# Performance work log

Measured on AMD Instinct MI355X. Metric: run time of the kernel, lower is better.

The kernel has to match this reference:

```python
import jax, jax.numpy as jnp
import numpy as np

B, T, D, H, E, O = 4, 2048, 512, 2048, 4, 512
C = 1024  # expert capacity
HE = H // E  # per-expert hidden width


def setup_inputs() -> dict:
    key = jax.random.key(0)
    ks = jax.random.split(key, 7)
    x = jax.random.normal(ks[0], (B, T, D), dtype=jnp.float32)
    dispatch_mask = jax.random.uniform(ks[1], (B, T, E, C), dtype=jnp.float32)
    combine_array = jax.random.uniform(ks[2], (B, T, E, C), dtype=jnp.float32)
    # per-expert parameters (fc1 contract, fc2 expand)
    w1 = jax.random.normal(ks[3], (E, D, HE), dtype=jnp.float32) * (1.0 / np.sqrt(D))
    b1 = jnp.zeros((E, HE), dtype=jnp.float32)
    w2 = jax.random.normal(ks[4], (E, HE, O), dtype=jnp.float32) * (1.0 / np.sqrt(HE))
    b2 = jnp.zeros((O,), dtype=jnp.float32)
    return {"x": x, "dispatch_mask": dispatch_mask, "combine_array": combine_array,
            "w1": w1, "b1": b1, "w2": w2, "b2": b2}


def reference(x, dispatch_mask, combine_array, w1, b1, w2, b2):
    # dispatch: gather tokens into per-expert capacity buffers [B,E,C,D]
    xd = jnp.einsum('btd,btec->becd', x, dispatch_mask)
    # per-expert fc1: [B,E,C,HE]
    h = jnp.einsum('becd,edh->bech', xd, w1) + b1[None, :, None, :]
    # GELU (exact erf form, matching torch nn.GELU default); norm/dropout are identity
    h = jax.nn.gelu(h, approximate=False)
    # per-expert fc2: [B,E,C,O]
    y = jnp.einsum('bech,eho->beco', h, w2)
    # combine: scatter expert outputs back to tokens [B,T,O]
    out = jnp.einsum('beco,btec->bto', y, combine_array) + b2
    return out
```

## Files before the change

### kernel.cpp

```cpp
#include <hip/hip_runtime.h>
#include <math.h>

namespace {

typedef short short8 __attribute__((ext_vector_type(8)));
typedef int i32x4 __attribute__((ext_vector_type(4)));
typedef float f32x4 __attribute__((ext_vector_type(4)));

constexpr int kB = 4, kT = 2048, kD = 512, kE = 4, kC = 1024, kHE = 512,
              kO = 512, kEC = 4096;

__device__ __forceinline__ unsigned short f2bf(float f) {
    unsigned int u = __float_as_uint(f);
    u += 0x7fffu + ((u >> 16) & 1u);
    return (unsigned short)(u >> 16);
}

__device__ __forceinline__ float gelu_exact(float v) {
    return 0.5f * v * (1.0f + erff(v * 0.70710678118654752f));
}

#define GLDS16(g, l)                                                      \
    __builtin_amdgcn_global_load_lds(                                     \
        (const __attribute__((address_space(1))) unsigned int*)(g),       \
        (__attribute__((address_space(3))) unsigned int*)(l), 16, 0, 0)

__global__ __launch_bounds__(256)
void transpose_cast(const float* __restrict__ in, unsigned short* __restrict__ out,
                    int R, int Cc, long long sIn, long long sOut)
{
    __shared__ float tile[32][33];
    const int z = blockIdx.z;
    const float* ip = in + (long long)z * sIn;
    unsigned short* op = out + (long long)z * sOut;
    const int c0 = blockIdx.x * 32, r0 = blockIdx.y * 32;
    const int tx = threadIdx.x & 31, ty = threadIdx.x >> 5;
#pragma unroll
    for (int i = 0; i < 4; ++i) {
        const int r = ty + i * 8;
        tile[r][tx] = ip[(size_t)(r0 + r) * Cc + c0 + tx];
    }
    __syncthreads();
#pragma unroll
    for (int i = 0; i < 4; ++i) {
        const int c = ty + i * 8;
        op[(size_t)(c0 + c) * R + r0 + tx] = f2bf(tile[tx][c]);
    }
}

__global__ __launch_bounds__(256)
void cast_bf16(const float* __restrict__ in, unsigned short* __restrict__ out,
               long long n)
{
    const long long i = ((long long)blockIdx.x * blockDim.x + threadIdx.x) * 4;
    if (i < n) {
        const float4 v = *(const float4*)&in[i];
        unsigned short o[4] = {f2bf(v.x), f2bf(v.y), f2bf(v.z), f2bf(v.w)};
        *(uint2*)&out[i] = *(const uint2*)o;
    }
}

template <int MODE>
__global__ __launch_bounds__(256, 1)
void mfma_gemm(const unsigned short* __restrict__ Aall,
               const unsigned short* __restrict__ Ball,
               const float* __restrict__ biasAll,
               void* __restrict__ Call,
               int M, int N, int K,
               long long sA, long long sB, long long sC,
               int zModA, int zModB, int zModBias, int biasStride, int bShift)
{
    __shared__ unsigned short As[4][128 * 64];
    __shared__ unsigned short Bs[4][128 * 64];

    const int z = blockIdx.z;
    const unsigned short* Ab = Aall + (long long)(z % zModA) * sA;
    const unsigned short* Bb = Ball + (long long)(z % zModB) * sB;
    const float* bias =
        (MODE != 0) ? biasAll + (long long)(z % zModBias) * biasStride : nullptr;

    const int gx = gridDim.x;
    int lin = blockIdx.y * gx + blockIdx.x;
    const int nwg = gx * gridDim.y;
    if ((nwg & 7) == 0) {
        const int q = nwg >> 3;
        lin = (lin & 7) * q + (lin >> 3);
    }
    const int gxs = 31 - __clz(gx);
    const int bx = lin & (gx - 1);
    const int by = lin >> gxs;
    const int row0 = by * 128;
    const int colB = bx * 128;

    const int t = threadIdx.x;
    const int lane = t & 63;
    const int w = t >> 6;
    const int wrow = w * 32;
    const int l8r = lane >> 3;
    const int l8c = ((lane & 7) ^ l8r) * 8;

    const int wm = (w >> 1) * 64;
    const int wn = (w & 1) * 64;
    const int fr = lane & 15;
    const int fq = (lane >> 4) * 8;
    const int fsw = (fr & 7) * 8;

    const unsigned int bMask = (1u << bShift) - 1u;

    f32x4 acc[4][4] = {};

    const unsigned aB0 =
        (unsigned)(size_t)(const __attribute__((address_space(3))) unsigned short*)
            &As[0][0] +
        (unsigned)(((wm + fr) * 64 + (fq ^ fsw)) * 2);
    const unsigned bB0 =
        (unsigned)(size_t)(const __attribute__((address_space(3))) unsigned short*)
            &Bs[0][0] +
        (unsigned)(((wn + fr) * 64 + (fq ^ fsw)) * 2);

    struct FragSet { i32x4 a0[4], a1[4], b0[4], b1[4]; };
    FragSet R0, R1;

#define DSR0(d, a) asm volatile("ds_read_b128 %0, %1" : "=v"(d) : "v"(a))
#define DSR1(d, a) asm volatile("ds_read_b128 %0, %1 offset:2048" : "=v"(d) : "v"(a))
#define DSR2(d, a) asm volatile("ds_read_b128 %0, %1 offset:4096" : "=v"(d) : "v"(a))
#define DSR3(d, a) asm volatile("ds_read_b128 %0, %1 offset:6144" : "=v"(d) : "v"(a))

#define READ16(R, CB)                                                         \
    do {                                                                      \
        const unsigned A0c = aB0 + (CB) * 16384u, A1c = A0c ^ 64u;            \
        const unsigned B0c = bB0 + (CB) * 16384u, B1c = B0c ^ 64u;            \
        DSR0(R.a0[0], A0c); DSR1(R.a0[1], A0c); DSR2(R.a0[2], A0c); DSR3(R.a0[3], A0c); \
        DSR0(R.b0[0], B0c); DSR1(R.b0[1], B0c); DSR2(R.b0[2], B0c); DSR3(R.b0[3], B0c); \
        DSR0(R.a1[0], A1c); DSR1(R.a1[1], A1c); DSR2(R.a1[2], A1c); DSR3(R.a1[3], A1c); \
        DSR0(R.b1[0], B1c); DSR1(R.b1[1], B1c); DSR2(R.b1[2], B1c); DSR3(R.b1[3], B1c); \
    } while (0)

#define MFMA16(R)                                                             \
    do {                                                                      \
        _Pragma("unroll") for (int i_ = 0; i_ < 4; ++i_)                      \
            _Pragma("unroll") for (int j_ = 0; j_ < 4; ++j_)                  \
                acc[i_][j_] = __builtin_amdgcn_mfma_f32_16x16x32_bf16(        \
                    __builtin_bit_cast(short8, R.a0[i_]),                     \
                    __builtin_bit_cast(short8, R.b0[j_]), acc[i_][j_], 0, 0, 0); \
        _Pragma("unroll") for (int i_ = 0; i_ < 4; ++i_)                      \
            _Pragma("unroll") for (int j_ = 0; j_ < 4; ++j_)                  \
                acc[i_][j_] = __builtin_amdgcn_mfma_f32_16x16x32_bf16(        \
                    __builtin_bit_cast(short8, R.a1[i_]),                     \
                    __builtin_bit_cast(short8, R.b1[j_]), acc[i_][j_], 0, 0, 0); \
    } while (0)

#define STAGE(buf, k0)                                                        \
    do {                                                                      \
        _Pragma("unroll")                                                     \
        for (int r = 0; r < 4; ++r) {                                         \
            const int ar = row0 + wrow + r * 8 + l8r;                         \
            GLDS16(Ab + (size_t)ar * K + ((k0) + l8c),                        \
                   &As[buf][(wrow + r * 8) * 64]);                            \
            const int bn = colB + wrow + r * 8 + l8r;                         \
            const int gk = (k0) + l8c;                                        \
            const size_t boff =                                               \
                (((size_t)(gk >> bShift) * N + bn) << bShift) + (gk & bMask); \
            GLDS16(Bb + boff, &Bs[buf][(wrow + r * 8) * 64]);                 \
        }                                                                     \
    } while (0)

#define ITER_FULL(T, CBRD, CBST, Rmf, Rrd)                                    \
    do {                                                                      \
        STAGE(CBST, ((T) + 2) * 64);                                          \
        asm volatile("s_waitcnt vmcnt(8)" ::: "memory");                      \
        __builtin_amdgcn_s_barrier();                                         \
        READ16(Rrd, CBRD);                                                    \
        MFMA16(Rmf);                                                          \
        asm volatile("s_waitcnt lgkmcnt(0)" ::: "memory");                    \
        __builtin_amdgcn_sched_barrier(0);                                    \
    } while (0)

    const int nt = K / 64;

    STAGE(0, 0);
    STAGE(1, 64);
    asm volatile("s_waitcnt vmcnt(8)" ::: "memory");
    __builtin_amdgcn_s_barrier();
    READ16(R0, 0);
    asm volatile("s_waitcnt lgkmcnt(0)" ::: "memory");
    __builtin_amdgcn_sched_barrier(0);

    for (int t0 = 0; t0 + 4 < nt; t0 += 4) {
        ITER_FULL(t0 + 0, 1, 2, R0, R1);
        ITER_FULL(t0 + 1, 2, 3, R1, R0);
        ITER_FULL(t0 + 2, 3, 0, R0, R1);
        ITER_FULL(t0 + 3, 0, 1, R1, R0);
    }
    ITER_FULL(nt - 4, 1, 2, R0, R1);
    ITER_FULL(nt - 3, 2, 3, R1, R0);
    asm volatile("s_waitcnt vmcnt(0)" ::: "memory");
    __builtin_amdgcn_s_barrier();
    READ16(R1, 3);
    MFMA16(R0);
    asm volatile("s_waitcnt lgkmcnt(0)" ::: "memory");
    __builtin_amdgcn_sched_barrier(0);
    MFMA16(R1);

#undef ITER_FULL
#undef STAGE
#undef MFMA16
#undef READ16
#undef DSR0
#undef DSR1
#undef DSR2
#undef DSR3

    const long long cz = (long long)z * sC;
#pragma unroll
    for (int i = 0; i < 4; ++i) {
        const int rowb = row0 + wm + i * 16 + (lane >> 4) * 4;
#pragma unroll
        for (int j = 0; j < 4; ++j) {
            const int col = colB + wn + j * 16 + fr;
            const float bv = (MODE != 0) ? bias[col] : 0.0f;
#pragma unroll
            for (int r = 0; r < 4; ++r) {
                const float v = acc[i][j][r];
                const size_t idx = (size_t)cz + (size_t)(rowb + r) * N + col;
                if (MODE == 0)
                    ((unsigned short*)Call)[idx] = f2bf(v);
                else if (MODE == 1)
                    ((unsigned short*)Call)[idx] = f2bf(gelu_exact(v + bv));
                else
                    ((float*)Call)[idx] = v + bv;
            }
        }
    }
}

}

extern "C" void kernel_launch(void* const* d_in, const int* in_sizes, int n_in,
                              void* d_out, int out_size, void* d_ws, size_t ws_size,
                              hipStream_t stream)
{
    const float* x    = (const float*)d_in[0];
    const float* mask = (const float*)d_in[1];
    const float* comb = (const float*)d_in[2];
    const float* w1   = (const float*)d_in[3];
    const float* b1   = (const float*)d_in[4];
    const float* w2   = (const float*)d_in[5];
    const float* b2   = (const float*)d_in[6];
    float* out = (float*)d_out;

    unsigned short* ws    = (unsigned short*)d_ws;
    unsigned short* regA  = ws;
    unsigned short* xT    = regA + 33554432;
    unsigned short* w1T   = xT + 4194304;
    unsigned short* w2T   = w1T + 1048576;
    unsigned short* xd    = w2T + 1048576;
    unsigned short* h     = xd + 8388608;
    unsigned short* maskT = regA;
    unsigned short* combB = regA;
    unsigned short* yT    = xd;

    dim3 blk(256);

    transpose_cast<<<dim3(kEC / 32, kT / 32, kB), blk, 0, stream>>>(
        mask, maskT, kT, kEC, (long long)kT * kEC, (long long)kT * kEC);
    transpose_cast<<<dim3(kD / 32, kT / 32, kB), blk, 0, stream>>>(
        x, xT, kT, kD, (long long)kT * kD, (long long)kT * kD);
    transpose_cast<<<dim3(kHE / 32, kD / 32, kE), blk, 0, stream>>>(
        w1, w1T, kD, kHE, (long long)kD * kHE, (long long)kD * kHE);
    transpose_cast<<<dim3(kO / 32, kHE / 32, kE), blk, 0, stream>>>(
        w2, w2T, kHE, kO, (long long)kHE * kO, (long long)kHE * kO);

    mfma_gemm<0><<<dim3(kD / 128, kEC / 128, kB), blk, 0, stream>>>(
        maskT, xT, nullptr, xd, kEC, kD, kT,
        (long long)kEC * kT, (long long)kD * kT, (long long)kEC * kD,
        kB, kB, 1, 0, 11);

    cast_bf16<<<dim3(33554432 / 4 / 256), blk, 0, stream>>>(
        comb, combB, 33554432LL);

    mfma_gemm<1><<<dim3(kHE / 128, kC / 128, kB * kE), blk, 0, stream>>>(
        xd, w1T, b1, h, kC, kHE, kD,
        (long long)kC * kD, (long long)kHE * kD, (long long)kC * kHE,
        kB * kE, kE, kE, kHE, 9);

    mfma_gemm<0><<<dim3(kC / 128, kO / 128, kB * kE), blk, 0, stream>>>(
        w2T, h, nullptr, yT, kO, kC, kHE,
        (long long)kO * kHE, (long long)kC * kHE, (long long)kO * kC,
        kE, kB * kE, 1, 0, 9);

    mfma_gemm<3><<<dim3(kO / 128, kT / 128, kB), blk, 0, stream>>>(
        combB, yT, b2, out, kT, kO, kEC,
        (long long)kT * kEC, (long long)kE * kO * kC, (long long)kT * kO,
        kB, kB, 1, 0, 10);
}
```

Measured before the change: 442.9 us.

## Fuse input conversions into one launch and deepen GEMM prefetch to three stages

Merges the four transpose-cast kernels and, when the workspace is large enough, the combine-array cast into a single flat-grid kernel. This removes several launches and the serialization between them. It also changes the 4-buffer LDS ring in the MFMA GEMM from a prefetch distance of two tiles to three, with adjusted vmcnt waits and a new epilogue, to hide more global-load latency. The fused path relies on a separate combB buffer, so it only runs when the workspace size check passes. Otherwise it falls back to the old cast kernel.

```diff
diff --git a/kernel.cpp b/kernel.cpp
--- a/kernel.cpp
+++ b/kernel.cpp
@@ -25,15 +25,11 @@
         (const __attribute__((address_space(1))) unsigned int*)(g),       \
         (__attribute__((address_space(3))) unsigned int*)(l), 16, 0, 0)
 
-__global__ __launch_bounds__(256)
-void transpose_cast(const float* __restrict__ in, unsigned short* __restrict__ out,
-                    int R, int Cc, long long sIn, long long sOut)
-{
-    __shared__ float tile[32][33];
-    const int z = blockIdx.z;
-    const float* ip = in + (long long)z * sIn;
-    unsigned short* op = out + (long long)z * sOut;
-    const int c0 = blockIdx.x * 32, r0 = blockIdx.y * 32;
+__device__ __forceinline__ void tc_body(float (*tile)[33],
+                                        const float* __restrict__ ip,
+                                        unsigned short* __restrict__ op,
+                                        int R, int Cc, int c0, int r0)
+{
     const int tx = threadIdx.x & 31, ty = threadIdx.x >> 5;
 #pragma unroll
     for (int i = 0; i < 4; ++i) {
@@ -45,6 +41,43 @@
     for (int i = 0; i < 4; ++i) {
         const int c = ty + i * 8;
         op[(size_t)(c0 + c) * R + r0 + tx] = f2bf(tile[tx][c]);
+    }
+}
+
+__global__ __launch_bounds__(256)
+void convert_all(const float* __restrict__ mask, unsigned short* __restrict__ maskT,
+                 const float* __restrict__ x, unsigned short* __restrict__ xT,
+                 const float* __restrict__ w1, unsigned short* __restrict__ w1T,
+                 const float* __restrict__ w2, unsigned short* __restrict__ w2T,
+                 const float* __restrict__ comb, unsigned short* __restrict__ combB)
+{
+    __shared__ float tile[32][33];
+    const int bid = blockIdx.x;
+    if (bid < 32768) {
+        const int txi = bid & 127, tyi = (bid >> 7) & 63, z = bid >> 13;
+        tc_body(tile, mask + (long long)z * kT * kEC,
+                maskT + (long long)z * kT * kEC, kT, kEC, txi * 32, tyi * 32);
+    } else if (bid < 36864) {
+        const int b2 = bid - 32768;
+        const int txi = b2 & 15, tyi = (b2 >> 4) & 63, z = b2 >> 10;
+        tc_body(tile, x + (long long)z * kT * kD,
+                xT + (long long)z * kT * kD, kT, kD, txi * 32, tyi * 32);
+    } else if (bid < 37888) {
+        const int b3 = bid - 36864;
+        const int txi = b3 & 15, tyi = (b3 >> 4) & 15, z = b3 >> 8;
+        tc_body(tile, w1 + (long long)z * kD * kHE,
+                w1T + (long long)z * kD * kHE, kD, kHE, txi * 32, tyi * 32);
+    } else if (bid < 38912) {
+        const int b4 = bid - 37888;
+        const int txi = b4 & 15, tyi = (b4 >> 4) & 15, z = b4 >> 8;
+        tc_body(tile, w2 + (long long)z * kHE * kO,
+                w2T + (long long)z * kHE * kO, kHE, kO, txi * 32, tyi * 32);
+    } else {
+        const long long i =
+            ((long long)(bid - 38912) * 256 + threadIdx.x) * 4;
+        const float4 v = *(const float4*)&comb[i];
+        unsigned short o[4] = {f2bf(v.x), f2bf(v.y), f2bf(v.z), f2bf(v.w)};
+        *(uint2*)&combB[i] = *(const uint2*)o;
     }
 }
 
@@ -167,8 +200,8 @@
 
 #define ITER_FULL(T, CBRD, CBST, Rmf, Rrd)                                    \
     do {                                                                      \
-        STAGE(CBST, ((T) + 2) * 64);                                          \
-        asm volatile("s_waitcnt vmcnt(8)" ::: "memory");                      \
+        STAGE(CBST, ((T) + 3) * 64);                                          \
+        asm volatile("s_waitcnt vmcnt(16)" ::: "memory");                     \
         __builtin_amdgcn_s_barrier();                                         \
         READ16(Rrd, CBRD);                                                    \
         MFMA16(Rmf);                                                          \
@@ -180,20 +213,26 @@
 
     STAGE(0, 0);
     STAGE(1, 64);
-    asm volatile("s_waitcnt vmcnt(8)" ::: "memory");
+    STAGE(2, 128);
+    asm volatile("s_waitcnt vmcnt(16)" ::: "memory");
     __builtin_amdgcn_s_barrier();
     READ16(R0, 0);
     asm volatile("s_waitcnt lgkmcnt(0)" ::: "memory");
     __builtin_amdgcn_sched_barrier(0);
 
-    for (int t0 = 0; t0 + 4 < nt; t0 += 4) {
-        ITER_FULL(t0 + 0, 1, 2, R0, R1);
-        ITER_FULL(t0 + 1, 2, 3, R1, R0);
-        ITER_FULL(t0 + 2, 3, 0, R0, R1);
-        ITER_FULL(t0 + 3, 0, 1, R1, R0);
-    }
-    ITER_FULL(nt - 4, 1, 2, R0, R1);
-    ITER_FULL(nt - 3, 2, 3, R1, R0);
+    for (int t0 = 0; t0 + 7 < nt; t0 += 4) {
+        ITER_FULL(t0 + 0, 1, 3, R0, R1);
+        ITER_FULL(t0 + 1, 2, 0, R1, R0);
+        ITER_FULL(t0 + 2, 3, 1, R0, R1);
+        ITER_FULL(t0 + 3, 0, 2, R1, R0);
+    }
+    ITER_FULL(nt - 4, 1, 3, R0, R1);
+    asm volatile("s_waitcnt vmcnt(8)" ::: "memory");
+    __builtin_amdgcn_s_barrier();
+    READ16(R0, 2);
+    MFMA16(R1);
+    asm volatile("s_waitcnt lgkmcnt(0)" ::: "memory");
+    __builtin_amdgcn_sched_barrier(0);
     asm volatile("s_waitcnt vmcnt(0)" ::: "memory");
     __builtin_amdgcn_s_barrier();
     READ16(R1, 3);
@@ -257,27 +296,25 @@
     unsigned short* xd    = w2T + 1048576;
     unsigned short* h     = xd + 8388608;
     unsigned short* maskT = regA;
-    unsigned short* combB = regA;
     unsigned short* yT    = xd;
 
+    const bool bigWs = ws_size >= (size_t)180355072;
+    unsigned short* combB = bigWs ? (h + 8388608) : regA;
+
     dim3 blk(256);
 
-    transpose_cast<<<dim3(kEC / 32, kT / 32, kB), blk, 0, stream>>>(
-        mask, maskT, kT, kEC, (long long)kT * kEC, (long long)kT * kEC);
-    transpose_cast<<<dim3(kD / 32, kT / 32, kB), blk, 0, stream>>>(
-        x, xT, kT, kD, (long long)kT * kD, (long long)kT * kD);
-    transpose_cast<<<dim3(kHE / 32, kD / 32, kE), blk, 0, stream>>>(
-        w1, w1T, kD, kHE, (long long)kD * kHE, (long long)kD * kHE);
-    transpose_cast<<<dim3(kO / 32, kHE / 32, kE), blk, 0, stream>>>(
-        w2, w2T, kHE, kO, (long long)kHE * kO, (long long)kHE * kO);
+    convert_all<<<dim3(bigWs ? 71680 : 38912), blk, 0, stream>>>(
+        mask, maskT, x, xT, w1, w1T, w2, w2T, comb, combB);
 
     mfma_gemm<0><<<dim3(kD / 128, kEC / 128, kB), blk, 0, stream>>>(
         maskT, xT, nullptr, xd, kEC, kD, kT,
         (long long)kEC * kT, (long long)kD * kT, (long long)kEC * kD,
         kB, kB, 1, 0, 11);
 
-    cast_bf16<<<dim3(33554432 / 4 / 256), blk, 0, stream>>>(
-        comb, combB, 33554432LL);
+    if (!bigWs) {
+        cast_bf16<<<dim3(33554432 / 4 / 256), blk, 0, stream>>>(
+            comb, combB, 33554432LL);
+    }
 
     mfma_gemm<1><<<dim3(kHE / 128, kC / 128, kB * kE), blk, 0, stream>>>(
         xd, w1T, b1, h, kC, kHE, kD,
```

Measured after the change: 461.8 us. 1.04x slower.

## Deepen GEMM prefetch to three stages, interleave LDS reads with MFMAs, widen transpose stores

Applied to the files above, without the earlier changes.

The GEMM main loop now prefetches three K-tiles ahead instead of two, using all four LDS buffers. Each iteration splits the fragment reads into four groups, each followed by eight MFMAs, so LDS latency hides behind matrix math. The transpose kernel now handles 64-row tiles and writes two packed bf16 values per 32-bit store to cut store count. The risks are a more fragile pipeline tail and rigid sched_barriers that may limit the compiler's own scheduling.

```diff
diff --git a/kernel.cpp b/kernel.cpp
--- a/kernel.cpp
+++ b/kernel.cpp
@@ -29,14 +29,14 @@
 void transpose_cast(const float* __restrict__ in, unsigned short* __restrict__ out,
                     int R, int Cc, long long sIn, long long sOut)
 {
-    __shared__ float tile[32][33];
+    __shared__ float tile[64][33];
     const int z = blockIdx.z;
     const float* ip = in + (long long)z * sIn;
     unsigned short* op = out + (long long)z * sOut;
-    const int c0 = blockIdx.x * 32, r0 = blockIdx.y * 32;
+    const int c0 = blockIdx.x * 32, r0 = blockIdx.y * 64;
     const int tx = threadIdx.x & 31, ty = threadIdx.x >> 5;
 #pragma unroll
-    for (int i = 0; i < 4; ++i) {
+    for (int i = 0; i < 8; ++i) {
         const int r = ty + i * 8;
         tile[r][tx] = ip[(size_t)(r0 + r) * Cc + c0 + tx];
     }
@@ -44,7 +44,9 @@
 #pragma unroll
     for (int i = 0; i < 4; ++i) {
         const int c = ty + i * 8;
-        op[(size_t)(c0 + c) * R + r0 + tx] = f2bf(tile[tx][c]);
+        const unsigned lo = f2bf(tile[tx * 2][c]);
+        const unsigned hi = f2bf(tile[tx * 2 + 1][c]);
+        *(unsigned*)&op[(size_t)(c0 + c) * R + r0 + tx * 2] = lo | (hi << 16);
     }
 }
 
@@ -126,28 +128,34 @@
 #define DSR2(d, a) asm volatile("ds_read_b128 %0, %1 offset:4096" : "=v"(d) : "v"(a))
 #define DSR3(d, a) asm volatile("ds_read_b128 %0, %1 offset:6144" : "=v"(d) : "v"(a))
 
+#define READ4(arr, addr)                                                      \
+    do {                                                                      \
+        DSR0((arr)[0], (addr)); DSR1((arr)[1], (addr));                       \
+        DSR2((arr)[2], (addr)); DSR3((arr)[3], (addr));                       \
+    } while (0)
+
+#define MFMA8(Aarr, Barr, ilo)                                                \
+    do {                                                                      \
+        _Pragma("unroll") for (int i_ = (ilo); i_ < (ilo) + 2; ++i_)          \
+            _Pragma("unroll") for (int j_ = 0; j_ < 4; ++j_)                  \
+                acc[i_][j_] = __builtin_amdgcn_mfma_f32_16x16x32_bf16(        \
+                    __builtin_bit_cast(short8, (Aarr)[i_]),                   \
+                    __builtin_bit_cast(short8, (Barr)[j_]), acc[i_][j_],      \
+                    0, 0, 0);                                                 \
+    } while (0)
+
 #define READ16(R, CB)                                                         \
     do {                                                                      \
         const unsigned A0c = aB0 + (CB) * 16384u, A1c = A0c ^ 64u;            \
         const unsigned B0c = bB0 + (CB) * 16384u, B1c = B0c ^ 64u;            \
-        DSR0(R.a0[0], A0c); DSR1(R.a0[1], A0c); DSR2(R.a0[2], A0c); DSR3(R.a0[3], A0c); \
-        DSR0(R.b0[0], B0c); DSR1(R.b0[1], B0c); DSR2(R.b0[2], B0c); DSR3(R.b0[3], B0c); \
-        DSR0(R.a1[0], A1c); DSR1(R.a1[1], A1c); DSR2(R.a1[2], A1c); DSR3(R.a1[3], A1c); \
-        DSR0(R.b1[0], B1c); DSR1(R.b1[1], B1c); DSR2(R.b1[2], B1c); DSR3(R.b1[3], B1c); \
+        READ4(R.a0, A0c); READ4(R.b0, B0c);                                   \
+        READ4(R.a1, A1c); READ4(R.b1, B1c);                                   \
     } while (0)
 
 #define MFMA16(R)                                                             \
     do {                                                                      \
-        _Pragma("unroll") for (int i_ = 0; i_ < 4; ++i_)                      \
-            _Pragma("unroll") for (int j_ = 0; j_ < 4; ++j_)                  \
-                acc[i_][j_] = __builtin_amdgcn_mfma_f32_16x16x32_bf16(        \
-                    __builtin_bit_cast(short8, R.a0[i_]),                     \
-                    __builtin_bit_cast(short8, R.b0[j_]), acc[i_][j_], 0, 0, 0); \
-        _Pragma("unroll") for (int i_ = 0; i_ < 4; ++i_)                      \
-            _Pragma("unroll") for (int j_ = 0; j_ < 4; ++j_)                  \
-                acc[i_][j_] = __builtin_amdgcn_mfma_f32_16x16x32_bf16(        \
-                    __builtin_bit_cast(short8, R.a1[i_]),                     \
-                    __builtin_bit_cast(short8, R.b1[j_]), acc[i_][j_], 0, 0, 0); \
+        MFMA8(R.a0, R.b0, 0); MFMA8(R.a0, R.b0, 2);                           \
+        MFMA8(R.a1, R.b1, 0); MFMA8(R.a1, R.b1, 2);                           \
     } while (0)
 
 #define STAGE(buf, k0)                                                        \
@@ -167,11 +175,26 @@
 
 #define ITER_FULL(T, CBRD, CBST, Rmf, Rrd)                                    \
     do {                                                                      \
-        STAGE(CBST, ((T) + 2) * 64);                                          \
-        asm volatile("s_waitcnt vmcnt(8)" ::: "memory");                      \
+        STAGE(CBST, ((T) + 3) * 64);                                          \
+        asm volatile("s_waitcnt vmcnt(16)" ::: "memory");                     \
         __builtin_amdgcn_s_barrier();                                         \
-        READ16(Rrd, CBRD);                                                    \
-        MFMA16(Rmf);                                                          \
+        const unsigned A0c_ = aB0 + (CBRD) * 16384u, A1c_ = A0c_ ^ 64u;       \
+        const unsigned B0c_ = bB0 + (CBRD) * 16384u, B1c_ = B0c_ ^ 64u;       \
+        READ4(Rrd.a0, A0c_);                                                  \
+        __builtin_amdgcn_sched_barrier(0);                                    \
+        MFMA8(Rmf.a0, Rmf.b0, 0);                                             \
+        __builtin_amdgcn_sched_barrier(0);                                    \
+        READ4(Rrd.b0, B0c_);                                                  \
+        __builtin_amdgcn_sched_barrier(0);                                    \
+        MFMA8(Rmf.a0, Rmf.b0, 2);                                             \
+        __builtin_amdgcn_sched_barrier(0);                                    \
+        READ4(Rrd.a1, A1c_);                                                  \
+        __builtin_amdgcn_sched_barrier(0);                                    \
+        MFMA8(Rmf.a1, Rmf.b1, 0);                                             \
+        __builtin_amdgcn_sched_barrier(0);                                    \
+        READ4(Rrd.b1, B1c_);                                                  \
+        __builtin_amdgcn_sched_barrier(0);                                    \
+        MFMA8(Rmf.a1, Rmf.b1, 2);                                             \
         asm volatile("s_waitcnt lgkmcnt(0)" ::: "memory");                    \
         __builtin_amdgcn_sched_barrier(0);                                    \
     } while (0)
@@ -180,20 +203,26 @@
 
     STAGE(0, 0);
     STAGE(1, 64);
-    asm volatile("s_waitcnt vmcnt(8)" ::: "memory");
+    STAGE(2, 128);
+    asm volatile("s_waitcnt vmcnt(16)" ::: "memory");
     __builtin_amdgcn_s_barrier();
     READ16(R0, 0);
     asm volatile("s_waitcnt lgkmcnt(0)" ::: "memory");
     __builtin_amdgcn_sched_barrier(0);
 
-    for (int t0 = 0; t0 + 4 < nt; t0 += 4) {
-        ITER_FULL(t0 + 0, 1, 2, R0, R1);
-        ITER_FULL(t0 + 1, 2, 3, R1, R0);
-        ITER_FULL(t0 + 2, 3, 0, R0, R1);
-        ITER_FULL(t0 + 3, 0, 1, R1, R0);
-    }
-    ITER_FULL(nt - 4, 1, 2, R0, R1);
-    ITER_FULL(nt - 3, 2, 3, R1, R0);
+    for (int t0 = 0; t0 + 7 < nt; t0 += 4) {
+        ITER_FULL(t0 + 0, 1, 3, R0, R1);
+        ITER_FULL(t0 + 1, 2, 0, R1, R0);
+        ITER_FULL(t0 + 2, 3, 1, R0, R1);
+        ITER_FULL(t0 + 3, 0, 2, R1, R0);
+    }
+    ITER_FULL(nt - 4, 1, 3, R0, R1);
+    asm volatile("s_waitcnt vmcnt(8)" ::: "memory");
+    __builtin_amdgcn_s_barrier();
+    READ16(R0, 2);
+    MFMA16(R1);
+    asm volatile("s_waitcnt lgkmcnt(0)" ::: "memory");
+    __builtin_amdgcn_sched_barrier(0);
     asm volatile("s_waitcnt vmcnt(0)" ::: "memory");
     __builtin_amdgcn_s_barrier();
     READ16(R1, 3);
@@ -206,6 +235,8 @@
 #undef STAGE
 #undef MFMA16
 #undef READ16
+#undef MFMA8
+#undef READ4
 #undef DSR0
 #undef DSR1
 #undef DSR2
@@ -262,13 +293,13 @@
 
     dim3 blk(256);
 
-    transpose_cast<<<dim3(kEC / 32, kT / 32, kB), blk, 0, stream>>>(
+    transpose_cast<<<dim3(kEC / 32, kT / 64, kB), blk, 0, stream>>>(
         mask, maskT, kT, kEC, (long long)kT * kEC, (long long)kT * kEC);
-    transpose_cast<<<dim3(kD / 32, kT / 32, kB), blk, 0, stream>>>(
+    transpose_cast<<<dim3(kD / 32, kT / 64, kB), blk, 0, stream>>>(
         x, xT, kT, kD, (long long)kT * kD, (long long)kT * kD);
-    transpose_cast<<<dim3(kHE / 32, kD / 32, kE), blk, 0, stream>>>(
+    transpose_cast<<<dim3(kHE / 32, kD / 64, kE), blk, 0, stream>>>(
         w1, w1T, kD, kHE, (long long)kD * kHE, (long long)kD * kHE);
-    transpose_cast<<<dim3(kO / 32, kHE / 32, kE), blk, 0, stream>>>(
+    transpose_cast<<<dim3(kO / 32, kHE / 64, kE), blk, 0, stream>>>(
         w2, w2T, kHE, kO, (long long)kHE * kO, (long long)kHE * kO);
 
     mfma_gemm<0><<<dim3(kD / 128, kEC / 128, kB), blk, 0, stream>>>(
```

New measurement: 442.6 us. Within noise of the previous version (-0.1%).

## Fuse all input transposes and combine cast into one conversion launch

Applied to the files above, without the earlier changes.

Merges the four transpose-cast launches and the combine-array bf16 cast into a single kernel that dispatches on block index. This is possible only when the workspace is big enough to give combB its own region instead of aliasing maskT. Each transpose block now covers 64 rows and writes two packed bf16 values per 32-bit store, giving wider stores and fewer launches. The cost is higher workspace use, plus a fallback path that runs when the workspace is smaller.

```diff
diff --git a/kernel.cpp b/kernel.cpp
--- a/kernel.cpp
+++ b/kernel.cpp
@@ -25,27 +25,72 @@
         (const __attribute__((address_space(1))) unsigned int*)(g),       \
         (__attribute__((address_space(3))) unsigned int*)(l), 16, 0, 0)
 
+__device__ __forceinline__ void tc_body(float (*tile)[33],
+                                        const float* __restrict__ ip,
+                                        unsigned short* __restrict__ op,
+                                        int R, int Cc, int c0, int r0)
+{
+    const int tx = threadIdx.x & 31, ty = threadIdx.x >> 5;
+#pragma unroll
+    for (int i = 0; i < 8; ++i) {
+        const int r = ty + i * 8;
+        tile[r][tx] = ip[(size_t)(r0 + r) * Cc + c0 + tx];
+    }
+    __syncthreads();
+#pragma unroll
+    for (int i = 0; i < 4; ++i) {
+        const int c = ty + i * 8;
+        const unsigned lo = f2bf(tile[tx * 2][c]);
+        const unsigned hi = f2bf(tile[tx * 2 + 1][c]);
+        *(unsigned*)&op[(size_t)(c0 + c) * R + r0 + tx * 2] = lo | (hi << 16);
+    }
+}
+
+__global__ __launch_bounds__(256)
+void convert_all(const float* __restrict__ mask, unsigned short* __restrict__ maskT,
+                 const float* __restrict__ x, unsigned short* __restrict__ xT,
+                 const float* __restrict__ w1, unsigned short* __restrict__ w1T,
+                 const float* __restrict__ w2, unsigned short* __restrict__ w2T,
+                 const float* __restrict__ comb, unsigned short* __restrict__ combB)
+{
+    __shared__ float tile[64][33];
+    const int bid = blockIdx.x;
+    if (bid < 16384) {
+        const int txi = bid & 127, tyi = (bid >> 7) & 31, z = bid >> 12;
+        tc_body(tile, mask + (long long)z * kT * kEC,
+                maskT + (long long)z * kT * kEC, kT, kEC, txi * 32, tyi * 64);
+    } else if (bid < 18432) {
+        const int b2 = bid - 16384;
+        const int txi = b2 & 15, tyi = (b2 >> 4) & 31, z = b2 >> 9;
+        tc_body(tile, x + (long long)z * kT * kD,
+                xT + (long long)z * kT * kD, kT, kD, txi * 32, tyi * 64);
+    } else if (bid < 18944) {
+        const int b3 = bid - 18432;
+        const int txi = b3 & 15, tyi = (b3 >> 4) & 7, z = b3 >> 7;
+        tc_body(tile, w1 + (long long)z * kD * kHE,
+                w1T + (long long)z * kD * kHE, kD, kHE, txi * 32, tyi * 64);
+    } else if (bid < 19456) {
+        const int b4 = bid - 18944;
+        const int txi = b4 & 15, tyi = (b4 >> 4) & 7, z = b4 >> 7;
+        tc_body(tile, w2 + (long long)z * kHE * kO,
+                w2T + (long long)z * kHE * kO, kHE, kO, txi * 32, tyi * 64);
+    } else {
+        const long long i =
+            ((long long)(bid - 19456) * 256 + threadIdx.x) * 4;
+        const float4 v = *(const float4*)&comb[i];
+        unsigned short o[4] = {f2bf(v.x), f2bf(v.y), f2bf(v.z), f2bf(v.w)};
+        *(uint2*)&combB[i] = *(const uint2*)o;
+    }
+}
+
 __global__ __launch_bounds__(256)
 void transpose_cast(const float* __restrict__ in, unsigned short* __restrict__ out,
                     int R, int Cc, long long sIn, long long sOut)
 {
-    __shared__ float tile[32][33];
+    __shared__ float tile[64][33];
     const int z = blockIdx.z;
-    const float* ip = in + (long long)z * sIn;
-    unsigned short* op = out + (long long)z * sOut;
-    const int c0 = blockIdx.x * 32, r0 = blockIdx.y * 32;
-    const int tx = threadIdx.x & 31, ty = threadIdx.x >> 5;
-#pragma unroll
-    for (int i = 0; i < 4; ++i) {
-        const int r = ty + i * 8;
-        tile[r][tx] = ip[(size_t)(r0 + r) * Cc + c0 + tx];
-    }
-    __syncthreads();
-#pragma unroll
-    for (int i = 0; i < 4; ++i) {
-        const int c = ty + i * 8;
-        op[(size_t)(c0 + c) * R + r0 + tx] = f2bf(tile[tx][c]);
-    }
+    tc_body(tile, in + (long long)z * sIn, out + (long long)z * sOut,
+            R, Cc, blockIdx.x * 32, blockIdx.y * 64);
 }
 
 __global__ __launch_bounds__(256)
@@ -257,27 +302,36 @@
     unsigned short* xd    = w2T + 1048576;
     unsigned short* h     = xd + 8388608;
     unsigned short* maskT = regA;
-    unsigned short* combB = regA;
     unsigned short* yT    = xd;
 
+    const bool bigWs = ws_size >= (size_t)180355072;
+    unsigned short* combB = bigWs ? (h + 8388608) : regA;
+
     dim3 blk(256);
 
-    transpose_cast<<<dim3(kEC / 32, kT / 32, kB), blk, 0, stream>>>(
-        mask, maskT, kT, kEC, (long long)kT * kEC, (long long)kT * kEC);
-    transpose_cast<<<dim3(kD / 32, kT / 32, kB), blk, 0, stream>>>(
-        x, xT, kT, kD, (long long)kT * kD, (long long)kT * kD);
-    transpose_cast<<<dim3(kHE / 32, kD / 32, kE), blk, 0, stream>>>(
-        w1, w1T, kD, kHE, (long long)kD * kHE, (long long)kD * kHE);
-    transpose_cast<<<dim3(kO / 32, kHE / 32, kE), blk, 0, stream>>>(
-        w2, w2T, kHE, kO, (long long)kHE * kO, (long long)kHE * kO);
+    if (bigWs) {
+        convert_all<<<dim3(52224), blk, 0, stream>>>(
+            mask, maskT, x, xT, w1, w1T, w2, w2T, comb, combB);
+    } else {
+        transpose_cast<<<dim3(kEC / 32, kT / 64, kB), blk, 0, stream>>>(
+            mask, maskT, kT, kEC, (long long)kT * kEC, (long long)kT * kEC);
+        transpose_cast<<<dim3(kD / 32, kT / 64, kB), blk, 0, stream>>>(
+            x, xT, kT, kD, (long long)kT * kD, (long long)kT * kD);
+        transpose_cast<<<dim3(kHE / 32, kD / 64, kE), blk, 0, stream>>>(
+            w1, w1T, kD, kHE, (long long)kD * kHE, (long long)kD * kHE);
+        transpose_cast<<<dim3(kO / 32, kHE / 64, kE), blk, 0, stream>>>(
+            w2, w2T, kHE, kO, (long long)kHE * kO, (long long)kHE * kO);
+    }
 
     mfma_gemm<0><<<dim3(kD / 128, kEC / 128, kB), blk, 0, stream>>>(
         maskT, xT, nullptr, xd, kEC, kD, kT,
         (long long)kEC * kT, (long long)kD * kT, (long long)kEC * kD,
         kB, kB, 1, 0, 11);
 
-    cast_bf16<<<dim3(33554432 / 4 / 256), blk, 0, stream>>>(
-        comb, combB, 33554432LL);
+    if (!bigWs) {
+        cast_bf16<<<dim3(33554432 / 4 / 256), blk, 0, stream>>>(
+            comb, combB, 33554432LL);
+    }
 
     mfma_gemm<1><<<dim3(kHE / 128, kC / 128, kB * kE), blk, 0, stream>>>(
         xd, w1T, b1, h, kC, kHE, kD,
```

Measured after the change: 474.3 us. 7.1% more time.
